# Performance work log

Measured on AMD Instinct MI355X. Metric: run time of the kernel, lower is better.

The kernel has to match this reference:

```python
import jax, jax.numpy as jnp
import numpy as np

N_SRC = 100000
N_DST = 20000
N_EDGES = 640000
D_IN = 128
D_OUT = 128


def setup_inputs() -> dict:
    key = jax.random.key(0)
    ks = jax.random.split(key, 6)
    feat_src = jax.random.normal(ks[0], (N_SRC, D_IN), dtype=jnp.float32)
    feat_dst = jax.random.normal(ks[1], (N_DST, D_IN), dtype=jnp.float32)
    src_idx = jax.random.randint(ks[2], (N_EDGES,), 0, N_SRC, dtype=jnp.int64 if jax.config.jax_enable_x64 else jnp.int32)
    dst_idx = jax.random.randint(ks[3], (N_EDGES,), 0, N_DST, dtype=jnp.int64 if jax.config.jax_enable_x64 else jnp.int32)
    # xavier-uniform-ish init scale for [out, in] Linear weights
    lim = float(np.sqrt(6.0 / (D_IN + D_OUT)))
    W_self = jax.random.uniform(ks[4], (D_OUT, D_IN), jnp.float32, -lim, lim)
    W_neigh = jax.random.uniform(ks[5], (D_OUT, D_IN), jnp.float32, -lim, lim)
    b_self = jnp.zeros((D_OUT,), jnp.float32)
    b_neigh = jnp.zeros((D_OUT,), jnp.float32)
    return {
        "feat_src": feat_src, "feat_dst": feat_dst,
        "src_idx": src_idx, "dst_idx": dst_idx,
        "W_self": W_self, "b_self": b_self,
        "W_neigh": W_neigh, "b_neigh": b_neigh,
    }


def reference(feat_src, feat_dst, src_idx, dst_idx, W_self, b_self, W_neigh, b_neigh):
    n_dst = feat_dst.shape[0]
    # message passing: copy_src + mean reduce over incoming edges per dst node
    msgs = feat_src[src_idx]                                   # [E, D_in]
    summed = jax.ops.segment_sum(msgs, dst_idx, num_segments=n_dst)  # [N_dst, D_in]
    deg = jax.ops.segment_sum(jnp.ones((src_idx.shape[0],), feat_src.dtype),
                              dst_idx, num_segments=n_dst)     # [N_dst]
    h_neigh = summed / jnp.maximum(deg, 1.0)[:, None]          # mean (0 for isolated)
    # rst = fc_self(h_self) + fc_neigh(h_neigh); no activation
    rst = (feat_dst @ W_self.T + b_self) + (h_neigh @ W_neigh.T + b_neigh)
    return rst
```

## Files before the change

kernel.cpp:

```cpp
#include <hip/hip_runtime.h>

#define D 128
#define NDST 20000
#define NHB 64
#define CAP 96

typedef __attribute__((ext_vector_type(8))) short short8;
typedef __attribute__((ext_vector_type(4))) float f32x4;
typedef __attribute__((ext_vector_type(2))) float f32x2;

__device__ __forceinline__ unsigned f2bf(float f) {
  unsigned x = __float_as_uint(f);
  return (x + 0x7FFFu + ((x >> 16) & 1u)) >> 16;
}
__device__ __forceinline__ unsigned pack2(float a, float b) {
  return f2bf(a) | (f2bf(b) << 16);
}
__device__ __forceinline__ unsigned pack_fp8x4(float a, float b, float c, float d) {
  int v = 0;
  v = __builtin_amdgcn_cvt_pk_fp8_f32(a, b, v, false);
  v = __builtin_amdgcn_cvt_pk_fp8_f32(c, d, v, true);
  return (unsigned)v;
}

__global__ __launch_bounds__(512) void k1(
    const int* __restrict__ dst_idx,
    const float* __restrict__ feat_src,
    const float* __restrict__ feat_dst,
    const float* __restrict__ W_self,
    const float* __restrict__ b_self,
    const float* __restrict__ b_neigh,
    unsigned char* __restrict__ hist8,
    unsigned char* __restrict__ rank8,
    unsigned char* __restrict__ fsrc8,
    float* __restrict__ out,
    int n_src, int n_dst, int n_edges, int EPB, int NCB)
{
  __shared__ __align__(16) unsigned char ldsb[43520];
  const int tid = threadIdx.x;
  const int bid = blockIdx.x;

  if (bid < NHB) {
    unsigned int* hist = reinterpret_cast<unsigned int*>(ldsb);
    for (int i = tid; i < NDST / 16; i += 512)
      reinterpret_cast<uint4*>(hist)[i] = make_uint4(0u, 0u, 0u, 0u);
    __syncthreads();
    const int e0 = bid * EPB;
    const int e1 = min(e0 + EPB, n_edges);
    for (int e = e0 + tid; e < e1; e += 512) {
      int d = dst_idx[e];
      int sh = (d & 3) << 3;
      unsigned old = atomicAdd(&hist[d >> 2], 1u << sh);
      rank8[e] = (unsigned char)((old >> sh) & 0xFFu);
    }
    __syncthreads();
    uint4* rowp = reinterpret_cast<uint4*>(hist8 + (size_t)bid * NDST);
    const uint4* h4 = reinterpret_cast<const uint4*>(hist);
    for (int i = tid; i < NDST / 16; i += 512) rowp[i] = h4[i];
  } else if (bid < NHB + NCB) {
    const long long NCONV = (long long)n_src * 16;
    const long long NU = NCONV + 16;
    const long long stride = (long long)NCB * 512;
    long long u = (long long)(bid - NHB) * 512 + tid;
    for (; u < NU; u += stride) {
      if (u < NCONV) {
        long long e = u * 8;
        const float4* p = reinterpret_cast<const float4*>(feat_src + e);
        float4 a = p[0], b = p[1];
        uint2 o;
        o.x = pack_fp8x4(a.x, a.y, a.z, a.w);
        o.y = pack_fp8x4(b.x, b.y, b.z, b.w);
        *reinterpret_cast<uint2*>(fsrc8 + e) = o;
      } else {
        *reinterpret_cast<uint2*>(fsrc8 + (size_t)n_src * D + (u - NCONV) * 8) =
            make_uint2(0u, 0u);
      }
    }
  } else {
    unsigned short (*As)[136] = reinterpret_cast<unsigned short (*)[136]>(ldsb);
    unsigned short (*Bs)[136] =
        reinterpret_cast<unsigned short (*)[136]>(ldsb + 32 * 136 * 2);
    const int w = tid >> 6;
    const int lane = tid & 63;
    const int row0 = (bid - NHB - NCB) * 32;

    {
      int r = tid >> 4;
      int q = tid & 15;
      int gr = row0 + r;
      uint4 o = make_uint4(0u, 0u, 0u, 0u);
      if (gr < n_dst) {
        const float4* p = reinterpret_cast<const float4*>(
            feat_dst + (size_t)gr * D + q * 8);
        float4 a = p[0], b = p[1];
        o.x = pack2(a.x, a.y); o.y = pack2(a.z, a.w);
        o.z = pack2(b.x, b.y); o.w = pack2(b.z, b.w);
      }
      *reinterpret_cast<uint4*>(&As[r][q * 8]) = o;
    }
    {
      int n = tid >> 2;
      int q = tid & 3;
      const float4* p = reinterpret_cast<const float4*>(
          W_self + (size_t)n * D + q * 32);
      #pragma unroll
      for (int h = 0; h < 4; ++h) {
        float4 a = p[2 * h], b = p[2 * h + 1];
        uint4 o;
        o.x = pack2(a.x, a.y); o.y = pack2(a.z, a.w);
        o.z = pack2(b.x, b.y); o.w = pack2(b.z, b.w);
        *reinterpret_cast<uint4*>(&Bs[n][q * 32 + h * 8]) = o;
      }
    }
    __syncthreads();

    const int m  = w & 1;
    const int n0 = (w >> 1) * 2;
    const int ar = m * 16 + (lane & 15);
    const int kb = (lane >> 4) * 8;
    f32x4 acc2[2];
    acc2[0] = (f32x4){0.f, 0.f, 0.f, 0.f};
    acc2[1] = (f32x4){0.f, 0.f, 0.f, 0.f};
    #pragma unroll
    for (int kh = 0; kh < 4; ++kh) {
      short8 a = *reinterpret_cast<const short8*>(&As[ar][kh * 32 + kb]);
      #pragma unroll
      for (int t2 = 0; t2 < 2; ++t2) {
        short8 b = *reinterpret_cast<const short8*>(
            &Bs[(n0 + t2) * 16 + (lane & 15)][kh * 32 + kb]);
        acc2[t2] = __builtin_amdgcn_mfma_f32_16x16x32_bf16(a, b, acc2[t2], 0, 0, 0);
      }
    }
    const int r0 = row0 + m * 16 + (lane >> 4) * 4;
    #pragma unroll
    for (int t2 = 0; t2 < 2; ++t2) {
      int col = (n0 + t2) * 16 + (lane & 15);
      float bv = b_self[col] + b_neigh[col];
      #pragma unroll
      for (int r = 0; r < 4; ++r) {
        int gr = r0 + r;
        if (gr < n_dst) out[(size_t)gr * D + col] = acc2[t2][r] + bv;
      }
    }
  }
}

__global__ __launch_bounds__(256) void pB(
    unsigned char* __restrict__ hist8,
    int* __restrict__ degi,
    int n_dst)
{
  int d = blockIdx.x * 256 + threadIdx.x;
  if (d >= n_dst) return;
  unsigned char* col = hist8 + d;
  unsigned run = 0;
  #pragma unroll 8
  for (int b = 0; b < NHB; ++b) {
    unsigned h = col[(size_t)b * NDST];
    col[(size_t)b * NDST] = (unsigned char)run;
    run += h;
  }
  degi[d] = (int)run;
}

__global__ __launch_bounds__(256) void p3(
    const int* __restrict__ src_idx,
    const int* __restrict__ dst_idx,
    const unsigned char* __restrict__ rank8,
    const unsigned char* __restrict__ blockBase8,
    int* __restrict__ bucket,
    int n_edges, int EPB)
{
  int e0 = (blockIdx.x * 256 + threadIdx.x) * 8;
  if (e0 >= n_edges) return;
  if (e0 + 8 <= n_edges) {
    int4 sa = *reinterpret_cast<const int4*>(src_idx + e0);
    int4 sb = *reinterpret_cast<const int4*>(src_idx + e0 + 4);
    int4 da = *reinterpret_cast<const int4*>(dst_idx + e0);
    int4 db = *reinterpret_cast<const int4*>(dst_idx + e0 + 4);
    uchar4 ra = *reinterpret_cast<const uchar4*>(rank8 + e0);
    uchar4 rb = *reinterpret_cast<const uchar4*>(rank8 + e0 + 4);
    int ds[8] = {da.x, da.y, da.z, da.w, db.x, db.y, db.z, db.w};
    int ss[8] = {sa.x, sa.y, sa.z, sa.w, sb.x, sb.y, sb.z, sb.w};
    unsigned rr[8] = {ra.x, ra.y, ra.z, ra.w, rb.x, rb.y, rb.z, rb.w};
    unsigned base[8];
    #pragma unroll
    for (int j = 0; j < 8; ++j) {
      int hb = (e0 + j) / EPB;
      base[j] = (unsigned)blockBase8[(size_t)hb * NDST + ds[j]];
    }
    #pragma unroll
    for (int j = 0; j < 8; ++j) {
      unsigned slot = base[j] + rr[j];
      if (slot < CAP) bucket[(size_t)ds[j] * CAP + slot] = ss[j];
    }
  } else {
    for (int e = e0; e < n_edges; ++e) {
      int d = dst_idx[e];
      int hb = e / EPB;
      unsigned slot = (unsigned)blockBase8[(size_t)hb * NDST + d] + rank8[e];
      if (slot < CAP) bucket[(size_t)d * CAP + slot] = src_idx[e];
    }
  }
}

__global__ __launch_bounds__(512) void tail(
    const unsigned char* __restrict__ fsrc8,
    const int* __restrict__ degi,
    const int* __restrict__ bucket,
    const float* __restrict__ W_neigh,
    float* __restrict__ out,
    int n_src, int n_dst)
{
  __shared__ unsigned short Ah[32][136];
  __shared__ unsigned short Bs[128][136];

  const int tid  = threadIdx.x;
  const int w    = tid >> 6;
  const int lane = tid & 63;
  const int row0 = blockIdx.x * 32;

  {
    int n = tid >> 2;
    int q = tid & 3;
    const float4* p = reinterpret_cast<const float4*>(
        W_neigh + (size_t)n * D + q * 32);
    #pragma unroll
    for (int h = 0; h < 4; ++h) {
      float4 a = p[2 * h], b = p[2 * h + 1];
      uint4 o;
      o.x = pack2(a.x, a.y); o.y = pack2(a.z, a.w);
      o.z = pack2(b.x, b.y); o.w = pack2(b.z, b.w);
      *reinterpret_cast<uint4*>(&Bs[n][q * 32 + h * 8]) = o;
    }
  }

  {
    const int g = lane >> 4;
    const int c = lane & 15;
    const uint2* fs2 = reinterpret_cast<const uint2*>(fsrc8);

    for (int it = 0; it < 4; ++it) {
      int row = w * 4 + it;
      int gr = row0 + row;
      if (gr >= n_dst) {
        if (lane < 16)
          *reinterpret_cast<uint4*>(&Ah[row][c * 8]) = make_uint4(0u,0u,0u,0u);
        continue;
      }
      const int total = degi[gr];
      const int use = min(total, CAP);
      const int* brow = bucket + (size_t)gr * CAP;

      float acc[8];
      #pragma unroll
      for (int j = 0; j < 8; ++j) acc[j] = 0.f;

      for (int i = g; i < use; i += 32) {
        int s[8];
        #pragma unroll
        for (int k = 0; k < 8; ++k)
          s[k] = (i + 4 * k < use) ? brow[i + 4 * k] : n_src;
        uint2 v[8];
        #pragma unroll
        for (int k = 0; k < 8; ++k)
          v[k] = fs2[(size_t)s[k] * 16 + c];
        #pragma unroll
        for (int k = 0; k < 8; ++k) {
          f32x2 a0 = __builtin_amdgcn_cvt_pk_f32_fp8(v[k].x, false);
          f32x2 a1 = __builtin_amdgcn_cvt_pk_f32_fp8(v[k].x, true);
          f32x2 a2 = __builtin_amdgcn_cvt_pk_f32_fp8(v[k].y, false);
          f32x2 a3 = __builtin_amdgcn_cvt_pk_f32_fp8(v[k].y, true);
          acc[0] += a0.x; acc[1] += a0.y; acc[2] += a1.x; acc[3] += a1.y;
          acc[4] += a2.x; acc[5] += a2.y; acc[6] += a3.x; acc[7] += a3.y;
        }
      }

      #pragma unroll
      for (int j = 0; j < 8; ++j) {
        acc[j] += __shfl_xor(acc[j], 16);
        acc[j] += __shfl_xor(acc[j], 32);
      }

      if (lane < 16) {
        float inv = 1.0f / fmaxf((float)total, 1.0f);
        uint4 o;
        o.x = pack2(acc[0] * inv, acc[1] * inv);
        o.y = pack2(acc[2] * inv, acc[3] * inv);
        o.z = pack2(acc[4] * inv, acc[5] * inv);
        o.w = pack2(acc[6] * inv, acc[7] * inv);
        *reinterpret_cast<uint4*>(&Ah[row][c * 8]) = o;
      }
    }
  }
  __syncthreads();

  const int m  = w & 1;
  const int n0 = (w >> 1) * 2;
  const int ar = m * 16 + (lane & 15);
  const int kb = (lane >> 4) * 8;

  f32x4 acc2[2];
  acc2[0] = (f32x4){0.f, 0.f, 0.f, 0.f};
  acc2[1] = (f32x4){0.f, 0.f, 0.f, 0.f};

  #pragma unroll
  for (int kh = 0; kh < 4; ++kh) {
    short8 a = *reinterpret_cast<const short8*>(&Ah[ar][kh * 32 + kb]);
    #pragma unroll
    for (int t2 = 0; t2 < 2; ++t2) {
      short8 b = *reinterpret_cast<const short8*>(
          &Bs[(n0 + t2) * 16 + (lane & 15)][kh * 32 + kb]);
      acc2[t2] = __builtin_amdgcn_mfma_f32_16x16x32_bf16(a, b, acc2[t2], 0, 0, 0);
    }
  }

  const int r0 = row0 + m * 16 + (lane >> 4) * 4;
  #pragma unroll
  for (int t2 = 0; t2 < 2; ++t2) {
    int col = (n0 + t2) * 16 + (lane & 15);
    #pragma unroll
    for (int r = 0; r < 4; ++r) {
      int gr = r0 + r;
      if (gr < n_dst) {
        size_t idx = (size_t)gr * D + col;
        out[idx] = out[idx] + acc2[t2][r];
      }
    }
  }
}

extern "C" void kernel_launch(void* const* d_in, const int* in_sizes, int n_in,
                              void* d_out, int out_size, void* d_ws, size_t ws_size,
                              hipStream_t stream) {
  const float* feat_src = (const float*)d_in[0];
  const float* feat_dst = (const float*)d_in[1];
  const int*   src_idx  = (const int*)d_in[2];
  const int*   dst_idx  = (const int*)d_in[3];
  const float* W_self   = (const float*)d_in[4];
  const float* b_self   = (const float*)d_in[5];
  const float* W_neigh  = (const float*)d_in[6];
  const float* b_neigh  = (const float*)d_in[7];
  float* out = (float*)d_out;

  const int n_src   = in_sizes[0] / D;
  const int n_dst   = in_sizes[1] / D;
  const int n_edges = in_sizes[2];

  unsigned char* fsrc8 = (unsigned char*)d_ws;
  int* degi   = (int*)(fsrc8 + (size_t)(n_src + 1) * D);
  int* bucket = degi + NDST;
  unsigned char* rank8 = (unsigned char*)(bucket + (size_t)NDST * CAP);
  unsigned char* hist8 = rank8 + (((size_t)n_edges + 15) & ~(size_t)15);

  const int EPB = (n_edges + NHB - 1) / NHB;
  const int NCB = 256;
  const int NG  = (n_dst + 31) / 32;

  k1<<<NHB + NCB + NG, 512, 0, stream>>>(
      dst_idx, feat_src, feat_dst, W_self, b_self, b_neigh,
      hist8, rank8, fsrc8, out, n_src, n_dst, n_edges, EPB, NCB);

  pB<<<(n_dst + 255) / 256, 256, 0, stream>>>(hist8, degi, n_dst);

  p3<<<(n_edges / 8 + 255) / 256, 256, 0, stream>>>(
      src_idx, dst_idx, rank8, hist8, bucket, n_edges, EPB);

  tail<<<NG, 512, 0, stream>>>(
      fsrc8, degi, bucket, W_neigh, out, n_src, n_dst);
}
```

Baseline: 62.70 us.

## Double dst rows per block and give each 16-lane group its own row

Both the self-projection GEMM blocks in k1 and the tail kernel now handle 64 destination rows per block instead of 32, so each block converts and stages W into LDS half as often and each wave computes four MFMA column tiles instead of two. In tail, each 16-lane group now gathers a whole destination row on its own instead of four groups splitting one row, which removes the cross-group shuffle reduction. The cost is fewer blocks, which may lower occupancy and parallelism on the gather, plus more LDS per block. Per-lane work now scales with each row's degree, so load balance across lanes depends on the degree spread.

```diff
diff --git a/kernel.cpp b/kernel.cpp
--- a/kernel.cpp
+++ b/kernel.cpp
@@ -36,7 +36,7 @@
     float* __restrict__ out,
     int n_src, int n_dst, int n_edges, int EPB, int NCB)
 {
-  __shared__ __align__(16) unsigned char ldsb[43520];
+  __shared__ __align__(16) unsigned char ldsb[52224];
   const int tid = threadIdx.x;
   const int bid = blockIdx.x;
 
@@ -79,24 +79,27 @@
   } else {
     unsigned short (*As)[136] = reinterpret_cast<unsigned short (*)[136]>(ldsb);
     unsigned short (*Bs)[136] =
-        reinterpret_cast<unsigned short (*)[136]>(ldsb + 32 * 136 * 2);
+        reinterpret_cast<unsigned short (*)[136]>(ldsb + 64 * 136 * 2);
     const int w = tid >> 6;
     const int lane = tid & 63;
-    const int row0 = (bid - NHB - NCB) * 32;
+    const int row0 = (bid - NHB - NCB) * 64;
 
     {
-      int r = tid >> 4;
-      int q = tid & 15;
+      int r = tid >> 3;
+      int q = tid & 7;
       int gr = row0 + r;
-      uint4 o = make_uint4(0u, 0u, 0u, 0u);
+      uint4 o0 = make_uint4(0u,0u,0u,0u), o1 = o0;
       if (gr < n_dst) {
         const float4* p = reinterpret_cast<const float4*>(
-            feat_dst + (size_t)gr * D + q * 8);
-        float4 a = p[0], b = p[1];
-        o.x = pack2(a.x, a.y); o.y = pack2(a.z, a.w);
-        o.z = pack2(b.x, b.y); o.w = pack2(b.z, b.w);
-      }
-      *reinterpret_cast<uint4*>(&As[r][q * 8]) = o;
+            feat_dst + (size_t)gr * D + q * 16);
+        float4 a = p[0], b = p[1], cc = p[2], dd = p[3];
+        o0.x = pack2(a.x, a.y);   o0.y = pack2(a.z, a.w);
+        o0.z = pack2(b.x, b.y);   o0.w = pack2(b.z, b.w);
+        o1.x = pack2(cc.x, cc.y); o1.y = pack2(cc.z, cc.w);
+        o1.z = pack2(dd.x, dd.y); o1.w = pack2(dd.z, dd.w);
+      }
+      *reinterpret_cast<uint4*>(&As[r][q * 16]) = o0;
+      *reinterpret_cast<uint4*>(&As[r][q * 16 + 8]) = o1;
     }
     {
       int n = tid >> 2;
@@ -114,27 +117,27 @@
     }
     __syncthreads();
 
-    const int m  = w & 1;
-    const int n0 = (w >> 1) * 2;
+    const int m  = w & 3;
+    const int nh = w >> 2;
     const int ar = m * 16 + (lane & 15);
     const int kb = (lane >> 4) * 8;
-    f32x4 acc2[2];
-    acc2[0] = (f32x4){0.f, 0.f, 0.f, 0.f};
-    acc2[1] = (f32x4){0.f, 0.f, 0.f, 0.f};
+    f32x4 acc2[4];
+    #pragma unroll
+    for (int t = 0; t < 4; ++t) acc2[t] = (f32x4){0.f, 0.f, 0.f, 0.f};
     #pragma unroll
     for (int kh = 0; kh < 4; ++kh) {
       short8 a = *reinterpret_cast<const short8*>(&As[ar][kh * 32 + kb]);
       #pragma unroll
-      for (int t2 = 0; t2 < 2; ++t2) {
+      for (int t2 = 0; t2 < 4; ++t2) {
         short8 b = *reinterpret_cast<const short8*>(
-            &Bs[(n0 + t2) * 16 + (lane & 15)][kh * 32 + kb]);
+            &Bs[(nh * 4 + t2) * 16 + (lane & 15)][kh * 32 + kb]);
         acc2[t2] = __builtin_amdgcn_mfma_f32_16x16x32_bf16(a, b, acc2[t2], 0, 0, 0);
       }
     }
     const int r0 = row0 + m * 16 + (lane >> 4) * 4;
     #pragma unroll
-    for (int t2 = 0; t2 < 2; ++t2) {
-      int col = (n0 + t2) * 16 + (lane & 15);
+    for (int t2 = 0; t2 < 4; ++t2) {
+      int col = (nh * 4 + t2) * 16 + (lane & 15);
       float bv = b_self[col] + b_neigh[col];
       #pragma unroll
       for (int r = 0; r < 4; ++r) {
@@ -212,13 +215,13 @@
     float* __restrict__ out,
     int n_src, int n_dst)
 {
-  __shared__ unsigned short Ah[32][136];
+  __shared__ unsigned short Ah[64][136];
   __shared__ unsigned short Bs[128][136];
 
   const int tid  = threadIdx.x;
   const int w    = tid >> 6;
   const int lane = tid & 63;
-  const int row0 = blockIdx.x * 32;
+  const int row0 = blockIdx.x * 64;
 
   {
     int n = tid >> 2;
@@ -240,12 +243,12 @@
     const int c = lane & 15;
     const uint2* fs2 = reinterpret_cast<const uint2*>(fsrc8);
 
-    for (int it = 0; it < 4; ++it) {
-      int row = w * 4 + it;
+    #pragma unroll
+    for (int rr = 0; rr < 2; ++rr) {
+      int row = w * 8 + rr * 4 + g;
       int gr = row0 + row;
       if (gr >= n_dst) {
-        if (lane < 16)
-          *reinterpret_cast<uint4*>(&Ah[row][c * 8]) = make_uint4(0u,0u,0u,0u);
+        *reinterpret_cast<uint4*>(&Ah[row][c * 8]) = make_uint4(0u,0u,0u,0u);
         continue;
       }
       const int total = degi[gr];
@@ -256,11 +259,11 @@
       #pragma unroll
       for (int j = 0; j < 8; ++j) acc[j] = 0.f;
 
-      for (int i = g; i < use; i += 32) {
+      for (int i = 0; i < use; i += 8) {
         int s[8];
         #pragma unroll
         for (int k = 0; k < 8; ++k)
-          s[k] = (i + 4 * k < use) ? brow[i + 4 * k] : n_src;
+          s[k] = (i + k < use) ? brow[i + k] : n_src;
         uint2 v[8];
         #pragma unroll
         for (int k = 0; k < 8; ++k)
@@ -276,49 +279,41 @@
         }
       }
 
-      #pragma unroll
-      for (int j = 0; j < 8; ++j) {
-        acc[j] += __shfl_xor(acc[j], 16);
-        acc[j] += __shfl_xor(acc[j], 32);
-      }
-
-      if (lane < 16) {
-        float inv = 1.0f / fmaxf((float)total, 1.0f);
-        uint4 o;
-        o.x = pack2(acc[0] * inv, acc[1] * inv);
-        o.y = pack2(acc[2] * inv, acc[3] * inv);
-        o.z = pack2(acc[4] * inv, acc[5] * inv);
-        o.w = pack2(acc[6] * inv, acc[7] * inv);
-        *reinterpret_cast<uint4*>(&Ah[row][c * 8]) = o;
-      }
+      float inv = 1.0f / fmaxf((float)total, 1.0f);
+      uint4 o;
+      o.x = pack2(acc[0] * inv, acc[1] * inv);
+      o.y = pack2(acc[2] * inv, acc[3] * inv);
+      o.z = pack2(acc[4] * inv, acc[5] * inv);
+      o.w = pack2(acc[6] * inv, acc[7] * inv);
+      *reinterpret_cast<uint4*>(&Ah[row][c * 8]) = o;
     }
   }
   __syncthreads();
 
-  const int m  = w & 1;
-  const int n0 = (w >> 1) * 2;
+  const int m  = w & 3;
+  const int nh = w >> 2;
   const int ar = m * 16 + (lane & 15);
   const int kb = (lane >> 4) * 8;
 
-  f32x4 acc2[2];
-  acc2[0] = (f32x4){0.f, 0.f, 0.f, 0.f};
-  acc2[1] = (f32x4){0.f, 0.f, 0.f, 0.f};
+  f32x4 acc2[4];
+  #pragma unroll
+  for (int t = 0; t < 4; ++t) acc2[t] = (f32x4){0.f, 0.f, 0.f, 0.f};
 
   #pragma unroll
   for (int kh = 0; kh < 4; ++kh) {
     short8 a = *reinterpret_cast<const short8*>(&Ah[ar][kh * 32 + kb]);
     #pragma unroll
-    for (int t2 = 0; t2 < 2; ++t2) {
+    for (int t2 = 0; t2 < 4; ++t2) {
       short8 b = *reinterpret_cast<const short8*>(
-          &Bs[(n0 + t2) * 16 + (lane & 15)][kh * 32 + kb]);
+          &Bs[(nh * 4 + t2) * 16 + (lane & 15)][kh * 32 + kb]);
       acc2[t2] = __builtin_amdgcn_mfma_f32_16x16x32_bf16(a, b, acc2[t2], 0, 0, 0);
     }
   }
 
   const int r0 = row0 + m * 16 + (lane >> 4) * 4;
   #pragma unroll
-  for (int t2 = 0; t2 < 2; ++t2) {
-    int col = (n0 + t2) * 16 + (lane & 15);
+  for (int t2 = 0; t2 < 4; ++t2) {
+    int col = (nh * 4 + t2) * 16 + (lane & 15);
     #pragma unroll
     for (int r = 0; r < 4; ++r) {
       int gr = r0 + r;
@@ -355,7 +350,7 @@
 
   const int EPB = (n_edges + NHB - 1) / NHB;
   const int NCB = 256;
-  const int NG  = (n_dst + 31) / 32;
+  const int NG  = (n_dst + 63) / 64;
 
   k1<<<NHB + NCB + NG, 512, 0, stream>>>(
       dst_idx, feat_src, feat_dst, W_self, b_self, b_neigh,
```

Measured after the change: 64.11 us. 2.2% more time.
